# Optimization experiments

Hardware: AMD Instinct MI355X
Metric: run time of the kernel (lower is better)

The kernel has to match this reference:

```python
import jax, jax.numpy as jnp
import numpy as np

N_NODES = 50000
N_EDGES = 600000
D_OBJ = 128
D_REL = 128
D_OUT = 128


def setup_inputs() -> dict:
    key = jax.random.key(0)
    ks = jax.random.split(key, 7)
    s_obj = 1.0 / np.sqrt(D_OBJ)
    s_rel = 1.0 / np.sqrt(D_REL)
    return {
        "obj_vecs": jax.random.normal(ks[0], (N_NODES, D_OBJ), dtype=jnp.float32),
        "rel_vecs": jax.random.normal(ks[1], (N_EDGES, D_REL), dtype=jnp.float32),
        "edge_index": jax.random.randint(ks[2], (N_EDGES, 2), 0, N_NODES, dtype=jnp.int64),
        "W_obj": jax.random.normal(ks[3], (D_OUT, D_OBJ), dtype=jnp.float32) * s_obj,
        "b_obj": jax.random.normal(ks[4], (D_OUT,), dtype=jnp.float32) * s_obj,
        "W_rel": jax.random.normal(ks[5], (D_OUT, D_REL), dtype=jnp.float32) * s_rel,
        "b_rel": jax.random.normal(ks[6], (D_OUT,), dtype=jnp.float32) * s_rel,
    }


def reference(obj_vecs, rel_vecs, edge_index, W_obj, b_obj, W_rel, b_rel):
    # Per-node linear once ([N, d_out]) instead of twice per edge -- same math
    # since lin_obj(x_i) + lin_obj(x_j) = (x_i W^T + b) + (x_j W^T + b).
    obj_lin = obj_vecs @ W_obj.T + b_obj            # [N, d_out]
    rel_lin = rel_vecs @ W_rel.T + b_rel            # [E, d_out]
    src = edge_index[:, 0]
    dst = edge_index[:, 1]
    # message = relu(lin_obj(obj_i) + lin_rel(rel_k) + lin_obj(obj_j))
    msg = jax.nn.relu(obj_lin[src] + rel_lin + obj_lin[dst])  # [E, d_out]
    # aggr='add', flow source_to_target: scatter-add at target nodes (col 1)
    aggr = jax.ops.segment_sum(msg, dst, num_segments=obj_vecs.shape[0])
    return jax.nn.relu(aggr)
```

## Files before the change

### kernel.cpp

```cpp
#include <hip/hip_runtime.h>

#define N_NODES 50000
#define N_EDGES 600000
#define DD 128

typedef __attribute__((ext_vector_type(8))) short short8;
typedef __attribute__((ext_vector_type(4))) float f32x4;

__device__ __forceinline__ short f2bf(float f) {
    union { float f; unsigned u; } v; v.f = f;
    unsigned r = v.u + 0x7fffu + ((v.u >> 16) & 1u);
    return (short)(r >> 16);
}
__device__ __forceinline__ float bf2f(short s) {
    union { float f; unsigned u; } v; v.u = ((unsigned)(unsigned short)s) << 16;
    return v.f;
}
__device__ __forceinline__ float u2f(unsigned u) {
    union { float f; unsigned u; } v; v.u = u;
    return v.f;
}

__global__ __launch_bounds__(256) void k_lin(const float* __restrict__ X,
                                             const float* __restrict__ W,
                                             const float* __restrict__ bias,
                                             short* __restrict__ Y,
                                             int ntiles) {
    __shared__ __align__(16) short Wl[128 * 136];
    for (int i = threadIdx.x; i < 128 * 128; i += 256) {
        int n = i >> 7, k = i & 127;
        Wl[n * 136 + k] = f2bf(W[i]);
    }
    __syncthreads();

    const int wave = threadIdx.x >> 6;
    const int lane = threadIdx.x & 63;
    const int g = lane >> 4, ln = lane & 15;

    float bb[8];
#pragma unroll
    for (int nt = 0; nt < 8; ++nt) bb[nt] = bias[nt * 16 + ln];

    for (int t = blockIdx.x * 4 + wave; t < ntiles; t += gridDim.x * 4) {
        const float* xr = X + (size_t)(t * 16 + ln) * DD;
        short8 a[4];
#pragma unroll
        for (int ks = 0; ks < 4; ++ks) {
            const float* p = xr + ks * 32 + g * 8;
            float4 t0 = *(const float4*)p;
            float4 t1 = *(const float4*)(p + 4);
            short8 v;
            v[0] = f2bf(t0.x); v[1] = f2bf(t0.y); v[2] = f2bf(t0.z); v[3] = f2bf(t0.w);
            v[4] = f2bf(t1.x); v[5] = f2bf(t1.y); v[6] = f2bf(t1.z); v[7] = f2bf(t1.w);
            a[ks] = v;
        }
#pragma unroll
        for (int nt = 0; nt < 8; ++nt) {
            f32x4 acc = {0.f, 0.f, 0.f, 0.f};
#pragma unroll
            for (int ks = 0; ks < 4; ++ks) {
                short8 b = *(const short8*)&Wl[(nt * 16 + ln) * 136 + ks * 32 + g * 8];
                acc = __builtin_amdgcn_mfma_f32_16x16x32_bf16(a[ks], b, acc, 0, 0, 0);
            }
#pragma unroll
            for (int r = 0; r < 4; ++r)
                Y[(size_t)(t * 16 + g * 4 + r) * DD + nt * 16 + ln] = f2bf(acc[r] + bb[nt]);
        }
    }
}

__global__ __launch_bounds__(256) void k_zero_int(int* __restrict__ p, int n) {
    int i = blockIdx.x * 256 + threadIdx.x;
    if (i < n) p[i] = 0;
}

__global__ __launch_bounds__(256) void k_count(const int* __restrict__ EI,
                                               int* __restrict__ counts) {
    int e = blockIdx.x * 256 + threadIdx.x;
    if (e < N_EDGES) atomicAdd(&counts[EI[2 * e + 1]], 1);
}

__global__ __launch_bounds__(256) void k_scan1(const int* __restrict__ counts,
                                               int* __restrict__ scanned,
                                               int* __restrict__ bsum) {
    __shared__ int tmp[256];
    const int t = threadIdx.x;
    const int i = blockIdx.x * 256 + t;
    int v = (i < N_NODES) ? counts[i] : 0;
    tmp[t] = v;
    __syncthreads();
#pragma unroll
    for (int off = 1; off < 256; off <<= 1) {
        int x = (t >= off) ? tmp[t - off] : 0;
        __syncthreads();
        tmp[t] += x;
        __syncthreads();
    }
    if (i < N_NODES) scanned[i] = tmp[t] - v;
    if (t == 255) bsum[blockIdx.x] = tmp[255];
}

__global__ __launch_bounds__(256) void k_scan2(int* __restrict__ bsum, int nb) {
    __shared__ int tmp[256];
    const int t = threadIdx.x;
    int v = (t < nb) ? bsum[t] : 0;
    tmp[t] = v;
    __syncthreads();
#pragma unroll
    for (int off = 1; off < 256; off <<= 1) {
        int x = (t >= off) ? tmp[t - off] : 0;
        __syncthreads();
        tmp[t] += x;
        __syncthreads();
    }
    if (t < nb) bsum[t] = tmp[t] - v;
}

__global__ __launch_bounds__(256) void k_scan3(const int* __restrict__ scanned,
                                               const int* __restrict__ bsum,
                                               int* __restrict__ offsets,
                                               int* __restrict__ cursor) {
    int i = blockIdx.x * 256 + threadIdx.x;
    if (i < N_NODES) {
        int off = scanned[i] + bsum[blockIdx.x];
        offsets[i] = off;
        cursor[i] = off;
    }
    if (i == 0) offsets[N_NODES] = N_EDGES;
}

__global__ __launch_bounds__(256) void k_scatter(const int* __restrict__ EI,
                                                 int* __restrict__ cursor,
                                                 int2* __restrict__ sorted) {
    int e = blockIdx.x * 256 + threadIdx.x;
    if (e < N_EDGES) {
        int2 sd = *(const int2*)(EI + 2 * e);
        int pos = atomicAdd(&cursor[sd.y], 1);
        sorted[pos] = make_int2(e, sd.x);
    }
}

__global__ __launch_bounds__(256) void k_gather(const short* __restrict__ RL,
                                                const short* __restrict__ OL,
                                                const int2* __restrict__ sorted,
                                                const int* __restrict__ offs,
                                                float* __restrict__ out) {
    const int wave = threadIdx.x >> 6;
    const int lane = threadIdx.x & 63;
    const int v = blockIdx.x * 4 + wave;
    if (v >= N_NODES) return;

    const int r0 = offs[v], r1 = offs[v + 1];
    const int deg = r1 - r0;

    const unsigned odu = *(const unsigned*)(OL + (size_t)v * DD + 2 * lane);
    const float od0 = u2f(odu << 16), od1 = u2f(odu & 0xffff0000u);

    float a0 = 0.f, a1 = 0.f;
    const int2* sp = sorted + r0;

    for (int base = 0; base < deg; base += 64) {
        const int nn = min(64, deg - base);
        int2 mp = make_int2(0, 0);
        if (lane < nn) mp = sp[base + lane];

        int e = 0;
        for (; e + 8 <= nn; e += 8) {
            unsigned rl[8], sl[8];
#pragma unroll
            for (int j = 0; j < 8; ++j) {
                const int eid = __shfl(mp.x, e + j);
                const int src = __shfl(mp.y, e + j);
                rl[j] = *(const unsigned*)(RL + (size_t)eid * DD + 2 * lane);
                sl[j] = *(const unsigned*)(OL + (size_t)src * DD + 2 * lane);
            }
#pragma unroll
            for (int j = 0; j < 8; ++j) {
                a0 += fmaxf(u2f(rl[j] << 16) + u2f(sl[j] << 16) + od0, 0.f);
                a1 += fmaxf(u2f(rl[j] & 0xffff0000u) + u2f(sl[j] & 0xffff0000u) + od1, 0.f);
            }
        }
        for (; e < nn; ++e) {
            const int eid = __shfl(mp.x, e);
            const int src = __shfl(mp.y, e);
            const unsigned rlu = *(const unsigned*)(RL + (size_t)eid * DD + 2 * lane);
            const unsigned slu = *(const unsigned*)(OL + (size_t)src * DD + 2 * lane);
            a0 += fmaxf(u2f(rlu << 16) + u2f(slu << 16) + od0, 0.f);
            a1 += fmaxf(u2f(rlu & 0xffff0000u) + u2f(slu & 0xffff0000u) + od1, 0.f);
        }
    }

    float2 o;
    o.x = fmaxf(a0, 0.f);
    o.y = fmaxf(a1, 0.f);
    *(float2*)(out + (size_t)v * DD + 2 * lane) = o;
}

__global__ __launch_bounds__(256) void k_aggr(const float* __restrict__ RV,
                                              const int2* __restrict__ sorted,
                                              const int* __restrict__ offs,
                                              const float* __restrict__ W,
                                              const float* __restrict__ bias,
                                              const short* __restrict__ OL,
                                              float* __restrict__ out) {
    __shared__ __align__(16) short Wl[128 * 136];
    for (int i = threadIdx.x; i < 128 * 128; i += 256) {
        int n = i >> 7, k = i & 127;
        Wl[n * 136 + k] = f2bf(W[i]);
    }
    __syncthreads();

    const int wave = threadIdx.x >> 6;
    const int lane = threadIdx.x & 63;
    const int g = lane >> 4, ln = lane & 15;
    const int nWaves = gridDim.x * 4;

    float brel[8];
#pragma unroll
    for (int nt = 0; nt < 8; ++nt) brel[nt] = bias[nt * 16 + ln];

    for (int v = blockIdx.x * 4 + wave; v < N_NODES; v += nWaves) {
        const int r0 = offs[v], r1 = offs[v + 1];
        float od[8];
#pragma unroll
        for (int nt = 0; nt < 8; ++nt)
            od[nt] = bf2f(OL[(size_t)v * DD + nt * 16 + ln]);
        float p[8] = {0.f, 0.f, 0.f, 0.f, 0.f, 0.f, 0.f, 0.f};

        for (int base = r0; base < r1; base += 16) {
            int posl = base + ln;
            if (posl >= r1) posl = r1 - 1;
            const int e_ln = sorted[posl].x;
            const float* xr = RV + (size_t)e_ln * DD;
            short8 a[4];
#pragma unroll
            for (int ks = 0; ks < 4; ++ks) {
                const float* pp = xr + ks * 32 + g * 8;
                float4 t0 = *(const float4*)pp;
                float4 t1 = *(const float4*)(pp + 4);
                short8 vv;
                vv[0] = f2bf(t0.x); vv[1] = f2bf(t0.y); vv[2] = f2bf(t0.z); vv[3] = f2bf(t0.w);
                vv[4] = f2bf(t1.x); vv[5] = f2bf(t1.y); vv[6] = f2bf(t1.z); vv[7] = f2bf(t1.w);
                a[ks] = vv;
            }
            f32x4 acc[8];
#pragma unroll
            for (int nt = 0; nt < 8; ++nt) {
                acc[nt] = (f32x4){0.f, 0.f, 0.f, 0.f};
#pragma unroll
                for (int ks = 0; ks < 4; ++ks) {
                    short8 b = *(const short8*)&Wl[(nt * 16 + ln) * 136 + ks * 32 + g * 8];
                    acc[nt] = __builtin_amdgcn_mfma_f32_16x16x32_bf16(a[ks], b, acc[nt], 0, 0, 0);
                }
            }
#pragma unroll
            for (int r = 0; r < 4; ++r) {
                const int pos = base + g * 4 + r;
                if (pos < r1) {
                    const int src = sorted[pos].y;
                    const short* ps = OL + (size_t)src * DD + ln;
#pragma unroll
                    for (int nt = 0; nt < 8; ++nt) {
                        float m = acc[nt][r] + brel[nt] + bf2f(ps[nt * 16]) + od[nt];
                        p[nt] += fmaxf(m, 0.f);
                    }
                }
            }
        }
#pragma unroll
        for (int nt = 0; nt < 8; ++nt) {
            p[nt] += __shfl_xor(p[nt], 16);
            p[nt] += __shfl_xor(p[nt], 32);
        }
#pragma unroll
        for (int nt = 0; nt < 8; ++nt) {
            if ((nt >> 1) == g)
                out[(size_t)v * DD + nt * 16 + ln] = fmaxf(p[nt], 0.f);
        }
    }
}

extern "C" void kernel_launch(void* const* d_in, const int* in_sizes, int n_in,
                              void* d_out, int out_size, void* d_ws, size_t ws_size,
                              hipStream_t stream) {
    const float* obj = (const float*)d_in[0];
    const float* rel = (const float*)d_in[1];
    const int*   ei  = (const int*)d_in[2];
    const float* Wo  = (const float*)d_in[3];
    const float* bo  = (const float*)d_in[4];
    const float* Wr  = (const float*)d_in[5];
    const float* br  = (const float*)d_in[6];
    float* out = (float*)d_out;

    const int NB_E = (N_EDGES + 255) / 256;
    const int NB_N = (N_NODES + 255) / 256;

    const size_t RL_BYTES = (size_t)N_EDGES * DD * 2;
    const size_t FAST_NEED = 173000000;

    char* ws = (char*)d_ws;

    if (ws_size >= FAST_NEED) {
        short* RLb     = (short*)ws;
        short* OLb     = (short*)(ws + RL_BYTES);
        int2*  sorted  = (int2*)(ws + RL_BYTES + 12800000);
        int*   counts  = (int*)(ws + RL_BYTES + 17600000);
        int*   scanned = (int*)(ws + RL_BYTES + 17800192);
        int*   offsets = (int*)(ws + RL_BYTES + 18000896);
        int*   cursor  = (int*)(ws + RL_BYTES + 18201600);
        int*   bsum    = (int*)(ws + RL_BYTES + 18401792);

        k_zero_int<<<NB_N, 256, 0, stream>>>(counts, N_NODES);
        k_lin<<<782, 256, 0, stream>>>(obj, Wo, bo, OLb, N_NODES / 16);
        k_lin<<<2048, 256, 0, stream>>>(rel, Wr, br, RLb, N_EDGES / 16);
        k_count<<<NB_E, 256, 0, stream>>>(ei, counts);
        k_scan1<<<NB_N, 256, 0, stream>>>(counts, scanned, bsum);
        k_scan2<<<1, 256, 0, stream>>>(bsum, NB_N);
        k_scan3<<<NB_N, 256, 0, stream>>>(scanned, bsum, offsets, cursor);
        k_scatter<<<NB_E, 256, 0, stream>>>(ei, cursor, sorted);
        k_gather<<<(N_NODES + 3) / 4, 256, 0, stream>>>(RLb, OLb, sorted, offsets, out);
    } else {
        short* OLb     = (short*)ws;
        int2*  sorted  = (int2*)(ws + 12800000);
        int*   counts  = (int*)(ws + 17600000);
        int*   scanned = (int*)(ws + 17800192);
        int*   offsets = (int*)(ws + 18000896);
        int*   cursor  = (int*)(ws + 18201600);
        int*   bsum    = (int*)(ws + 18401792);

        k_zero_int<<<NB_N, 256, 0, stream>>>(counts, N_NODES);
        k_lin<<<782, 256, 0, stream>>>(obj, Wo, bo, OLb, N_NODES / 16);
        k_count<<<NB_E, 256, 0, stream>>>(ei, counts);
        k_scan1<<<NB_N, 256, 0, stream>>>(counts, scanned, bsum);
        k_scan2<<<1, 256, 0, stream>>>(bsum, NB_N);
        k_scan3<<<NB_N, 256, 0, stream>>>(scanned, bsum, offsets, cursor);
        k_scatter<<<NB_E, 256, 0, stream>>>(ei, cursor, sorted);
        k_aggr<<<2048, 256, 0, stream>>>(rel, sorted, offsets, Wr, br, OLb, out);
    }
}
```

Baseline: 270.2 us.

## Write edge linear outputs in destination-sorted order for contiguous gather reads

Moves the edge linear transform after the CSR sort and has it read rel_vecs rows through the sorted permutation, storing results in sorted edge order. The gather kernel then reads each edge's projected row contiguously from the node's CSR range instead of by random edge id. This trades random bf16 reads in the gather for random fp32 row reads in the linear kernel, and puts the edge linear on the critical path after the sort.

After: 278.2 us. 3.0% more time.

```diff
diff --git a/kernel.cpp b/kernel.cpp
--- a/kernel.cpp
+++ b/kernel.cpp
@@ -69,6 +69,56 @@
     }
 }
 
+__global__ __launch_bounds__(256) void k_lin_perm(const float* __restrict__ X,
+                                                  const int2* __restrict__ sorted,
+                                                  const float* __restrict__ W,
+                                                  const float* __restrict__ bias,
+                                                  short* __restrict__ Y,
+                                                  int ntiles) {
+    __shared__ __align__(16) short Wl[128 * 136];
+    for (int i = threadIdx.x; i < 128 * 128; i += 256) {
+        int n = i >> 7, k = i & 127;
+        Wl[n * 136 + k] = f2bf(W[i]);
+    }
+    __syncthreads();
+
+    const int wave = threadIdx.x >> 6;
+    const int lane = threadIdx.x & 63;
+    const int g = lane >> 4, ln = lane & 15;
+
+    float bb[8];
+#pragma unroll
+    for (int nt = 0; nt < 8; ++nt) bb[nt] = bias[nt * 16 + ln];
+
+    for (int t = blockIdx.x * 4 + wave; t < ntiles; t += gridDim.x * 4) {
+        const int eid = sorted[t * 16 + ln].x;
+        const float* xr = X + (size_t)eid * DD;
+        short8 a[4];
+#pragma unroll
+        for (int ks = 0; ks < 4; ++ks) {
+            const float* p = xr + ks * 32 + g * 8;
+            float4 t0 = *(const float4*)p;
+            float4 t1 = *(const float4*)(p + 4);
+            short8 v;
+            v[0] = f2bf(t0.x); v[1] = f2bf(t0.y); v[2] = f2bf(t0.z); v[3] = f2bf(t0.w);
+            v[4] = f2bf(t1.x); v[5] = f2bf(t1.y); v[6] = f2bf(t1.z); v[7] = f2bf(t1.w);
+            a[ks] = v;
+        }
+#pragma unroll
+        for (int nt = 0; nt < 8; ++nt) {
+            f32x4 acc = {0.f, 0.f, 0.f, 0.f};
+#pragma unroll
+            for (int ks = 0; ks < 4; ++ks) {
+                short8 b = *(const short8*)&Wl[(nt * 16 + ln) * 136 + ks * 32 + g * 8];
+                acc = __builtin_amdgcn_mfma_f32_16x16x32_bf16(a[ks], b, acc, 0, 0, 0);
+            }
+#pragma unroll
+            for (int r = 0; r < 4; ++r)
+                Y[(size_t)(t * 16 + g * 4 + r) * DD + nt * 16 + ln] = f2bf(acc[r] + bb[nt]);
+        }
+    }
+}
+
 __global__ __launch_bounds__(256) void k_zero_int(int* __restrict__ p, int n) {
     int i = blockIdx.x * 256 + threadIdx.x;
     if (i < n) p[i] = 0;
@@ -140,11 +190,11 @@
     }
 }
 
-__global__ __launch_bounds__(256) void k_gather(const short* __restrict__ RL,
-                                                const short* __restrict__ OL,
-                                                const int2* __restrict__ sorted,
-                                                const int* __restrict__ offs,
-                                                float* __restrict__ out) {
+__global__ __launch_bounds__(256) void k_gather2(const short* __restrict__ RLs,
+                                                 const short* __restrict__ OL,
+                                                 const int2* __restrict__ sorted,
+                                                 const int* __restrict__ offs,
+                                                 float* __restrict__ out) {
     const int wave = threadIdx.x >> 6;
     const int lane = threadIdx.x & 63;
     const int v = blockIdx.x * 4 + wave;
@@ -158,6 +208,7 @@
 
     float a0 = 0.f, a1 = 0.f;
     const int2* sp = sorted + r0;
+    const short* rp = RLs + (size_t)r0 * DD;
 
     for (int base = 0; base < deg; base += 64) {
         const int nn = min(64, deg - base);
@@ -168,10 +219,11 @@
         for (; e + 8 <= nn; e += 8) {
             unsigned rl[8], sl[8];
 #pragma unroll
+            for (int j = 0; j < 8; ++j)
+                rl[j] = *(const unsigned*)(rp + (size_t)(base + e + j) * DD + 2 * lane);
+#pragma unroll
             for (int j = 0; j < 8; ++j) {
-                const int eid = __shfl(mp.x, e + j);
                 const int src = __shfl(mp.y, e + j);
-                rl[j] = *(const unsigned*)(RL + (size_t)eid * DD + 2 * lane);
                 sl[j] = *(const unsigned*)(OL + (size_t)src * DD + 2 * lane);
             }
 #pragma unroll
@@ -181,9 +233,8 @@
             }
         }
         for (; e < nn; ++e) {
-            const int eid = __shfl(mp.x, e);
             const int src = __shfl(mp.y, e);
-            const unsigned rlu = *(const unsigned*)(RL + (size_t)eid * DD + 2 * lane);
+            const unsigned rlu = *(const unsigned*)(rp + (size_t)(base + e) * DD + 2 * lane);
             const unsigned slu = *(const unsigned*)(OL + (size_t)src * DD + 2 * lane);
             a0 += fmaxf(u2f(rlu << 16) + u2f(slu << 16) + od0, 0.f);
             a1 += fmaxf(u2f(rlu & 0xffff0000u) + u2f(slu & 0xffff0000u) + od1, 0.f);
@@ -301,7 +352,7 @@
     char* ws = (char*)d_ws;
 
     if (ws_size >= FAST_NEED) {
-        short* RLb     = (short*)ws;
+        short* RLs     = (short*)ws;
         short* OLb     = (short*)(ws + RL_BYTES);
         int2*  sorted  = (int2*)(ws + RL_BYTES + 12800000);
         int*   counts  = (int*)(ws + RL_BYTES + 17600000);
@@ -311,14 +362,14 @@
         int*   bsum    = (int*)(ws + RL_BYTES + 18401792);
 
         k_zero_int<<<NB_N, 256, 0, stream>>>(counts, N_NODES);
-        k_lin<<<782, 256, 0, stream>>>(obj, Wo, bo, OLb, N_NODES / 16);
-        k_lin<<<2048, 256, 0, stream>>>(rel, Wr, br, RLb, N_EDGES / 16);
         k_count<<<NB_E, 256, 0, stream>>>(ei, counts);
         k_scan1<<<NB_N, 256, 0, stream>>>(counts, scanned, bsum);
         k_scan2<<<1, 256, 0, stream>>>(bsum, NB_N);
         k_scan3<<<NB_N, 256, 0, stream>>>(scanned, bsum, offsets, cursor);
         k_scatter<<<NB_E, 256, 0, stream>>>(ei, cursor, sorted);
-        k_gather<<<(N_NODES + 3) / 4, 256, 0, stream>>>(RLb, OLb, sorted, offsets, out);
+        k_lin<<<782, 256, 0, stream>>>(obj, Wo, bo, OLb, N_NODES / 16);
+        k_lin_perm<<<2048, 256, 0, stream>>>(rel, sorted, Wr, br, RLs, N_EDGES / 16);
+        k_gather2<<<(N_NODES + 3) / 4, 256, 0, stream>>>(RLs, OLb, sorted, offsets, out);
     } else {
         short* OLb     = (short*)ws;
         int2*  sorted  = (int2*)(ws + 12800000);
```
